# Kernel tuning notes

Measured on AMD Instinct MI355X. Metric: run time of the kernel, lower is better.

## Reference

```python
import jax, jax.numpy as jnp
import numpy as np

B, T, E, H, D = 4, 2048, 1024, 16, 64


def setup_inputs() -> dict:
    key = jax.random.key(0)
    k1, k2, k3, k4 = jax.random.split(key, 4)
    s = 1.0 / np.sqrt(E)
    return {
        "x": jax.random.normal(k1, (B, T, E), dtype=jnp.float32),
        "wj_w": jax.random.uniform(k2, (E, E), jnp.float32, -s, s),   # torch Linear weight (out,in)
        "wjv_w": jax.random.uniform(k3, (E, E), jnp.float32, -s, s),
        "wo_w": jax.random.uniform(k4, (E, H * D), jnp.float32, -s, s),
    }


def reference(x, wj_w, wjv_w, wo_w):
    b, t, e = x.shape
    # echo = x @ wj_w.T ; eb = echo @ wj_w  (F.linear with transposed weight)
    eb = (x @ wj_w.T) @ wj_w
    sc = jnp.sum(x * eb, axis=-1) / jnp.sqrt(jnp.asarray(e, x.dtype))  # (B,T)
    # rank-1 outer-product scores with strict-upper causal mask
    ja = sc[:, :, None] * sc[:, None, :]                               # (B,T,T)
    causal = jnp.tril(jnp.ones((t, t), dtype=bool))
    ja = jnp.where(causal[None], ja, -jnp.inf)
    ja = jax.nn.softmax(ja, axis=-1)                                   # (B,T,T)
    # values per head; attention map shared across heads (broadcast, not materialized)
    val = (x @ wjv_w.T).reshape(b, t, H, D)                            # (B,T,H,D)
    out = jnp.einsum("bts,bshd->bthd", ja, val)                       # (B,T,H,D)
    return out.reshape(b, t, H * D) @ wo_w.T                           # (B,T,E)
```

## Files before the change

kernel.cpp:

```cpp
#include <hip/hip_runtime.h>
#include <math.h>

#define R_ROWS 8192
#define T_SEQ  2048
#define E_DIM  1024
#define KC     32
#define KCR    256
#define PBATCH_ELEMS ((size_t)4352 * 512)

typedef __attribute__((ext_vector_type(8))) short short8;
typedef __attribute__((ext_vector_type(4))) float f32x4;

__device__ __forceinline__ ushort f2bf(float f) {
  uint u = __float_as_uint(f);
  u += 0x7FFFu + ((u >> 16) & 1u);
  return (ushort)(u >> 16);
}
__device__ __forceinline__ float bf2f(ushort h) {
  return __uint_as_float(((uint)h) << 16);
}


__global__ __launch_bounds__(256) void cvt_split_frag(
    const float* __restrict__ in, ushort* __restrict__ hi,
    ushort* __restrict__ lo, int n)
{
  int g = blockIdx.x * 256 + threadIdx.x;
  if (g >= n) return;
  const int l = g & 15, h = (g >> 4) & 3;
  const int pq = g >> 6;
  const int q = pq & (KC - 1), p = pq >> 5;
  const size_t src = (size_t)(p * 16 + l) * 1024 + q * 32 + h * 8;
  const float4 v0 = *(const float4*)&in[src];
  const float4 v1 = *(const float4*)&in[src + 4];
  ushort hh[8], ll[8];
  const float v[8] = {v0.x, v0.y, v0.z, v0.w, v1.x, v1.y, v1.z, v1.w};
#pragma unroll
  for (int e = 0; e < 8; ++e) {
    hh[e] = f2bf(v[e]);
    ll[e] = f2bf(v[e] - bf2f(hh[e]));
  }
  *(uint4*)&hi[(size_t)g * 8] = *(const uint4*)hh;
  *(uint4*)&lo[(size_t)g * 8] = *(const uint4*)ll;
}

__global__ __launch_bounds__(256) void cvt_splitT_frag(
    const float* __restrict__ in, ushort* __restrict__ hi,
    ushort* __restrict__ lo, int n)
{
  int g = blockIdx.x * 256 + threadIdx.x;
  if (g >= n) return;
  const int l = g & 15, h = (g >> 4) & 3;
  const int pq = g >> 6;
  const int q = pq & (KC - 1), p = pq >> 5;
  const int rr = p * 16 + l;
  const int cc = q * 32 + h * 8;
  ushort hh[8], ll[8];
#pragma unroll
  for (int e = 0; e < 8; ++e) {
    const float v = in[(size_t)(cc + e) * 1024 + rr];
    hh[e] = f2bf(v);
    ll[e] = f2bf(v - bf2f(hh[e]));
  }
  *(uint4*)&hi[(size_t)g * 8] = *(const uint4*)hh;
  *(uint4*)&lo[(size_t)g * 8] = *(const uint4*)ll;
}

struct Frags { short8 ah[4], al[4], bh[4], bl[4]; };

__global__ __launch_bounds__(256, 2) void gemm_sq_direct(
    const ushort* __restrict__ xh, const ushort* __restrict__ xl,
    const ushort* __restrict__ wh, const ushort* __restrict__ wl,
    float* __restrict__ sc_raw)
{
  const int tid = threadIdx.x;
  const int m0 = blockIdx.y * 128, n0 = blockIdx.x * 128;
  const int wave = tid >> 6, lane = tid & 63;
  const int l15 = lane & 15, lq = lane >> 4;
  const int wm = (wave & 1) * 64, wn = (wave >> 1) * 64;

  size_t aoff[4], boff[4];
#pragma unroll
  for (int i = 0; i < 4; ++i)
    aoff[i] = ((size_t)(((m0 + wm) >> 4) + i) * KC * 4 + lq) * 128 + l15 * 8;
#pragma unroll
  for (int j = 0; j < 4; ++j)
    boff[j] = ((size_t)(((n0 + wn) >> 4) + j) * KC * 4 + lq) * 128 + l15 * 8;

  f32x4 acc[4][4] = {};
  Frags f0, f1;

  auto load = [&](Frags& f, int q) {
    const size_t dq = (size_t)q * 512;
#pragma unroll
    for (int i = 0; i < 4; ++i) {
      f.ah[i] = *(const short8*)(xh + aoff[i] + dq);
      f.al[i] = *(const short8*)(xl + aoff[i] + dq);
    }
#pragma unroll
    for (int j = 0; j < 4; ++j) {
      f.bh[j] = *(const short8*)(wh + boff[j] + dq);
      f.bl[j] = *(const short8*)(wl + boff[j] + dq);
    }
  };
  auto step = [&](const Frags& f) {
#pragma unroll
    for (int i = 0; i < 4; ++i)
#pragma unroll
      for (int j = 0; j < 4; ++j) {
        acc[i][j] = __builtin_amdgcn_mfma_f32_16x16x32_bf16(f.ah[i], f.bh[j], acc[i][j], 0, 0, 0);
        acc[i][j] = __builtin_amdgcn_mfma_f32_16x16x32_bf16(f.ah[i], f.bl[j], acc[i][j], 0, 0, 0);
        acc[i][j] = __builtin_amdgcn_mfma_f32_16x16x32_bf16(f.al[i], f.bh[j], acc[i][j], 0, 0, 0);
      }
  };

  load(f0, 0);
#pragma unroll 1
  for (int q = 0; q < KC; q += 2) {
    load(f1, q + 1);
    step(f0);
    if (q + 2 < KC) load(f0, q + 2);
    step(f1);
  }

  __shared__ float red[128][33];
#pragma unroll
  for (int i = 0; i < 4; ++i)
#pragma unroll
    for (int r = 0; r < 4; ++r) {
      const int row = wm + i * 16 + lq * 4 + r;
      float s = 0.f;
#pragma unroll
      for (int j = 0; j < 4; ++j) s += acc[i][j][r] * acc[i][j][r];
      red[row][(l15 << 1) | (wave >> 1)] = s;
    }
  __syncthreads();
  if (tid < 128) {
    float s = 0.f;
#pragma unroll
    for (int c = 0; c < 32; ++c) s += red[tid][c];
    atomicAdd(&sc_raw[m0 + tid], s);
  }
}

struct Frags2 { short8 ah[2], al[2], bh[2], bl[2]; };

__global__ __launch_bounds__(256, 2) void gemm_m_split(
    const ushort* __restrict__ ah_, const ushort* __restrict__ al_,
    const ushort* __restrict__ bh_, const ushort* __restrict__ bl_,
    ushort* __restrict__ Mf)
{
  const int tid = threadIdx.x;
  const int m0 = blockIdx.y * 64, n0 = blockIdx.x * 64;
  const int wave = tid >> 6, lane = tid & 63;
  const int l15 = lane & 15, lq = lane >> 4;
  const int wm = (wave & 1) * 32, wn = (wave >> 1) * 32;

  size_t aoff[2], boff[2];
#pragma unroll
  for (int i = 0; i < 2; ++i)
    aoff[i] = ((size_t)(((m0 + wm) >> 4) + i) * KC * 4 + lq) * 128 + l15 * 8;
#pragma unroll
  for (int j = 0; j < 2; ++j)
    boff[j] = ((size_t)(((n0 + wn) >> 4) + j) * KC * 4 + lq) * 128 + l15 * 8;

  f32x4 acc[2][2] = {};
  Frags2 f0, f1;

  auto load = [&](Frags2& f, int q) {
    const size_t dq = (size_t)q * 512;
#pragma unroll
    for (int i = 0; i < 2; ++i) {
      f.ah[i] = *(const short8*)(ah_ + aoff[i] + dq);
      f.al[i] = *(const short8*)(al_ + aoff[i] + dq);
    }
#pragma unroll
    for (int j = 0; j < 2; ++j) {
      f.bh[j] = *(const short8*)(bh_ + boff[j] + dq);
      f.bl[j] = *(const short8*)(bl_ + boff[j] + dq);
    }
  };
  auto step = [&](const Frags2& f) {
#pragma unroll
    for (int i = 0; i < 2; ++i)
#pragma unroll
      for (int j = 0; j < 2; ++j) {
        acc[i][j] = __builtin_amdgcn_mfma_f32_16x16x32_bf16(f.ah[i], f.bh[j], acc[i][j], 0, 0, 0);
        acc[i][j] = __builtin_amdgcn_mfma_f32_16x16x32_bf16(f.ah[i], f.bl[j], acc[i][j], 0, 0, 0);
        acc[i][j] = __builtin_amdgcn_mfma_f32_16x16x32_bf16(f.al[i], f.bh[j], acc[i][j], 0, 0, 0);
      }
  };

  load(f0, 0);
#pragma unroll 1
  for (int q = 0; q < KC; q += 2) {
    load(f1, q + 1);
    step(f0);
    if (q + 2 < KC) load(f0, q + 2);
    step(f1);
  }

#pragma unroll
  for (int i = 0; i < 2; ++i)
#pragma unroll
    for (int j = 0; j < 2; ++j) {
      const int fb = m0 + wm + i * 16 + lq * 4;
      const int k  = n0 + wn + j * 16 + l15;
#pragma unroll
      for (int r = 0; r < 4; ++r) {
        const int f = fb + r;
        const size_t addr =
            (((size_t)(f >> 4) * KC + (k >> 5)) * 4 + ((k >> 3) & 3)) * 128 +
            (f & 15) * 8 + (k & 7);
        Mf[addr] = f2bf(acc[i][j][r]);
      }
    }
}

__global__ __launch_bounds__(1024) void scan_max(
    const float* __restrict__ sc_raw, float* __restrict__ sc,
    float* __restrict__ pmax)
{
  const int b = blockIdx.x;
  __shared__ float b0[T_SEQ];
  __shared__ float b1[T_SEQ];
  const int tid = threadIdx.x;
  for (int i = tid; i < T_SEQ; i += 1024) {
    const float v = sc_raw[b*T_SEQ + i] * 0.03125f;
    b0[i] = v;
    sc[b*T_SEQ + i] = v;
  }
  __syncthreads();
  float* src = b0; float* dst = b1;
  for (int off = 1; off < T_SEQ; off <<= 1) {
    for (int i = tid; i < T_SEQ; i += 1024)
      dst[i] = (i >= off) ? fmaxf(src[i], src[i - off]) : src[i];
    __syncthreads();
    float* tmp = src; src = dst; dst = tmp;
  }
  for (int i = tid; i < T_SEQ; i += 1024) pmax[b*T_SEQ + i] = src[i];
}

__global__ __launch_bounds__(256) void zgen(
    const float* __restrict__ sc, const float* __restrict__ pmax,
    float* __restrict__ zinv)
{
  const int row = blockIdx.x * 4 + (threadIdx.x >> 6);
  const int lane = threadIdx.x & 63;
  const int t = row & (T_SEQ - 1);
  const int base = row & ~(T_SEQ - 1);
  const float st = sc[row], pm = pmax[row];
  float z = 0.f;
  for (int s = lane; s <= t; s += 64)
    z += __expf(st * (sc[base + s] - pm));
#pragma unroll
  for (int m = 1; m < 64; m <<= 1) z += __shfl_xor(z, m);
  if (lane == 0) zinv[row] = 1.0f / z;
}

__global__ __launch_bounds__(512) void pgen(
    const float* __restrict__ sc, const float* __restrict__ pmax,
    ushort* __restrict__ P012, ushort* __restrict__ P3)
{
  const int y = blockIdx.x, b = blockIdx.y, zslice = blockIdx.z;
  const int bT = b * T_SEQ;
  ushort* pb = (b < 3) ? P012 + (size_t)b * PBATCH_ELEMS : P3;
  __shared__ float scs[T_SEQ];
  __shared__ float pms[T_SEQ];
  const int tid = threadIdx.x;
  for (int i = tid; i < T_SEQ; i += 512) {
    scs[i] = sc[bT + i];
    pms[i] = pmax[bT + i];
  }
  __syncthreads();

#pragma unroll 1
  for (int ph = 0; ph < 2; ++ph) {
    const int P = ph ? y : 15 - y;
    const int W = 4 * P + 4;
    ushort* base = pb + (size_t)(16 * P * (P + 1)) * 512;
    const int nu = 512 * W;
#pragma unroll 1
    for (int u = tid + zslice * 512; u < nu; u += 2048) {
      const int sub = u & 63, hi = sub >> 4, l = sub & 15;
      const int pr = (u >> 6) & 7, q = u >> 9;
      const int t = P * 128 + pr * 16 + l;
      const int s0 = q * 32 + hi * 8;
      const float st = scs[t], pm = pms[t];
      ushort tmp[8];
#pragma unroll
      for (int e = 0; e < 8; ++e) {
        const int s = s0 + e;
        float pe = 0.f;
        if (s <= t) pe = __expf(st * (scs[s] - pm));
        tmp[e] = f2bf(pe);
      }
      *(uint4*)&base[(size_t)(pr * W + q) * 512 + hi * 128 + l * 8] =
          *(const uint4*)tmp;
    }
  }
}

struct FragsP { short8 a[4], b[4]; };

__global__ __launch_bounds__(256, 2) void gemm_wt(
    const ushort* __restrict__ Af, const ushort* __restrict__ Bf,
    ushort* __restrict__ WT)
{
  const int tid = threadIdx.x;
  const int m0 = blockIdx.y * 128, n0 = blockIdx.x * 128;
  const int wave = tid >> 6, lane = tid & 63;
  const int l15 = lane & 15, lq = lane >> 4;
  const int wm = (wave & 1) * 64, wn = (wave >> 1) * 64;

  size_t aoff[4], boff[4];
#pragma unroll
  for (int i = 0; i < 4; ++i)
    aoff[i] = ((size_t)(((m0 + wm) >> 4) + i) * KC * 4 + lq) * 128 + l15 * 8;
#pragma unroll
  for (int j = 0; j < 4; ++j)
    boff[j] = ((size_t)(((n0 + wn) >> 4) + j) * KC * 4 + lq) * 128 + l15 * 8;

  f32x4 acc[4][4] = {};
  FragsP f0, f1;

  auto load = [&](FragsP& f, int q) {
    const size_t dq = (size_t)q * 512;
#pragma unroll
    for (int i = 0; i < 4; ++i) f.a[i] = *(const short8*)(Af + aoff[i] + dq);
#pragma unroll
    for (int j = 0; j < 4; ++j) f.b[j] = *(const short8*)(Bf + boff[j] + dq);
  };
  auto step = [&](const FragsP& f) {
#pragma unroll
    for (int i = 0; i < 4; ++i)
#pragma unroll
      for (int j = 0; j < 4; ++j)
        acc[i][j] = __builtin_amdgcn_mfma_f32_16x16x32_bf16(f.a[i], f.b[j], acc[i][j], 0, 0, 0);
  };

  load(f0, 0);
#pragma unroll 1
  for (int q = 0; q < KC; q += 2) {
    load(f1, q + 1);
    step(f0);
    if (q + 2 < KC) load(f0, q + 2);
    step(f1);
  }

#pragma unroll
  for (int i = 0; i < 4; ++i)
#pragma unroll
    for (int j = 0; j < 4; ++j) {
      const int eb = m0 + wm + i * 16 + lq * 4;
      const int rg = n0 + wn + j * 16 + l15;
#pragma unroll
      for (int r = 0; r < 4; ++r) {
        const int e = eb + r;
        const size_t addr =
            (((size_t)(e >> 4) * KCR + (rg >> 5)) * 4 + ((rg >> 3) & 3)) * 128 +
            (e & 15) * 8 + (rg & 7);
        WT[addr] = f2bf(acc[i][j][r]);
      }
    }
}

__global__ __launch_bounds__(256, 2) void attn_gemm(
    const ushort* __restrict__ P012, const ushort* __restrict__ P3,
    const ushort* __restrict__ WT, const float* __restrict__ zinv,
    float* __restrict__ outp)
{
  const int b = blockIdx.z, y = blockIdx.y;
  const int e0 = blockIdx.x * 128;
  const int bT = b * T_SEQ;
  const ushort* pb = (b < 3) ? P012 + (size_t)b * PBATCH_ELEMS : P3;
  const int tid = threadIdx.x;
  const int wave = tid >> 6, lane = tid & 63;
  const int l15 = lane & 15, lq = lane >> 4;
  const int wm = (wave & 1) * 64, wn = (wave >> 1) * 64;

  size_t boff[4];
#pragma unroll
  for (int j = 0; j < 4; ++j)
    boff[j] = ((size_t)((((e0 + wn) >> 4) + j) * KCR + (bT >> 5)) * 4 + lq) * 128
              + l15 * 8;

#pragma unroll 1
  for (int ph = 0; ph < 2; ++ph) {
    const int ty = ph ? y : 15 - y;
    const int W = 4 * ty + 4;
    const int t0 = ty * 128;

    size_t aoff[4];
#pragma unroll
    for (int i = 0; i < 4; ++i)
      aoff[i] = ((size_t)(16 * ty * (ty + 1)) + (size_t)((wm >> 4) + i) * W) * 512
                + lq * 128 + l15 * 8;

    f32x4 acc[4][4] = {};
    FragsP f0, f1;

    auto load = [&](FragsP& f, int q) {
      const size_t dq = (size_t)q * 512;
#pragma unroll
      for (int i = 0; i < 4; ++i) f.a[i] = *(const short8*)(pb + aoff[i] + dq);
#pragma unroll
      for (int j = 0; j < 4; ++j) f.b[j] = *(const short8*)(WT + boff[j] + dq);
    };
    auto step = [&](const FragsP& f) {
#pragma unroll
      for (int i = 0; i < 4; ++i)
#pragma unroll
        for (int j = 0; j < 4; ++j)
          acc[i][j] = __builtin_amdgcn_mfma_f32_16x16x32_bf16(f.a[i], f.b[j], acc[i][j], 0, 0, 0);
    };

    load(f0, 0);
#pragma unroll 1
    for (int q = 0; q < W; q += 2) {
      load(f1, q + 1);
      step(f0);
      if (q + 2 < W) load(f0, q + 2);
      step(f1);
    }

#pragma unroll
    for (int i = 0; i < 4; ++i)
#pragma unroll
      for (int r = 0; r < 4; ++r) {
        const int row = t0 + wm + i * 16 + lq * 4 + r;
        const float zi = zinv[bT + row];
#pragma unroll
        for (int j = 0; j < 4; ++j) {
          const int nb = e0 + wn + j * 16 + l15;
          outp[(size_t)(bT + row) * E_DIM + nb] = acc[i][j][r] * zi;
        }
      }
  }
}

extern "C" void kernel_launch(void* const* d_in, const int* in_sizes, int n_in,
                              void* d_out, int out_size, void* d_ws, size_t ws_size,
                              hipStream_t stream) {
  (void)in_sizes; (void)n_in; (void)out_size; (void)ws_size;
  const float* x   = (const float*)d_in[0];
  const float* wj  = (const float*)d_in[1];
  const float* wjv = (const float*)d_in[2];
  const float* wo  = (const float*)d_in[3];
  float* out = (float*)d_out;

  ushort* xh_f  = (ushort*)d_ws;
  ushort* xl_f  = xh_f  + (size_t)R_ROWS * E_DIM;
  ushort* bufA  = xl_f  + (size_t)R_ROWS * E_DIM;
  ushort* bufB  = bufA  + (size_t)E_DIM * E_DIM;
  ushort* bufC  = bufB  + (size_t)E_DIM * E_DIM;
  ushort* bufD  = bufC  + (size_t)E_DIM * E_DIM;
  ushort* Mf    = bufD  + (size_t)E_DIM * E_DIM;
  float* sc_raw = (float*)(Mf + (size_t)E_DIM * E_DIM);
  float* sc     = sc_raw + R_ROWS;
  float* pmax   = sc + R_ROWS;
  float* zinv   = pmax + R_ROWS;
  ushort* WT    = xl_f;
  ushort* P012  = xh_f;
  ushort* P3    = bufA;

  hipMemsetAsync(sc_raw, 0, R_ROWS * sizeof(float), stream);

  cvt_split_frag <<<E_DIM*E_DIM/8/256, 256, 0, stream>>>(wo,  bufA, bufB, E_DIM*E_DIM/8);
  cvt_splitT_frag<<<E_DIM*E_DIM/8/256, 256, 0, stream>>>(wjv, bufC, bufD, E_DIM*E_DIM/8);
  gemm_m_split<<<dim3(E_DIM/64, E_DIM/64), 256, 0, stream>>>(bufA, bufB, bufC, bufD, Mf);

  cvt_split_frag<<<R_ROWS*E_DIM/8/256, 256, 0, stream>>>(x,  xh_f, xl_f, R_ROWS*E_DIM/8);
  cvt_split_frag<<<E_DIM*E_DIM/8/256, 256, 0, stream>>>(wj, bufA, bufB, E_DIM*E_DIM/8);

  gemm_sq_direct<<<dim3(E_DIM/128, R_ROWS/128), 256, 0, stream>>>(
      xh_f, xl_f, bufA, bufB, sc_raw);
  scan_max<<<4, 1024, 0, stream>>>(sc_raw, sc, pmax);
  zgen<<<R_ROWS/4, 256, 0, stream>>>(sc, pmax, zinv);

  gemm_wt<<<dim3(R_ROWS/128, E_DIM/128), 256, 0, stream>>>(Mf, xh_f, WT);

  pgen<<<dim3(8, 4, 4), 512, 0, stream>>>(sc, pmax, P012, P3);

  attn_gemm<<<dim3(E_DIM/128, 8, 4), 256, 0, stream>>>(P012, P3, WT, zinv, out);
}
```

Before: 275.2 us.

## Fuse weight conversions into one launch and widen attention GEMM to eight waves

Merges the three weight bf16 hi/lo split kernels into a single launch, giving each weight its own workspace buffers. The attention GEMM block grows from 4 to 8 waves, with each wave computing a 64x32 tile instead of 64x64. This aims to cut launch overhead and raise latency hiding and occupancy in the final GEMM. The trade-offs are extra workspace and more redundant loads of the A fragments per MFMA.

```diff
diff --git a/kernel.cpp b/kernel.cpp
--- a/kernel.cpp
+++ b/kernel.cpp
@@ -21,12 +21,10 @@
 }
 
 
-__global__ __launch_bounds__(256) void cvt_split_frag(
+__device__ __forceinline__ void split_frag_unit(
     const float* __restrict__ in, ushort* __restrict__ hi,
-    ushort* __restrict__ lo, int n)
-{
-  int g = blockIdx.x * 256 + threadIdx.x;
-  if (g >= n) return;
+    ushort* __restrict__ lo, int g)
+{
   const int l = g & 15, h = (g >> 4) & 3;
   const int pq = g >> 6;
   const int q = pq & (KC - 1), p = pq >> 5;
@@ -44,12 +42,10 @@
   *(uint4*)&lo[(size_t)g * 8] = *(const uint4*)ll;
 }
 
-__global__ __launch_bounds__(256) void cvt_splitT_frag(
+__device__ __forceinline__ void splitT_frag_unit(
     const float* __restrict__ in, ushort* __restrict__ hi,
-    ushort* __restrict__ lo, int n)
-{
-  int g = blockIdx.x * 256 + threadIdx.x;
-  if (g >= n) return;
+    ushort* __restrict__ lo, int g)
+{
   const int l = g & 15, h = (g >> 4) & 3;
   const int pq = g >> 6;
   const int q = pq & (KC - 1), p = pq >> 5;
@@ -64,6 +60,29 @@
   }
   *(uint4*)&hi[(size_t)g * 8] = *(const uint4*)hh;
   *(uint4*)&lo[(size_t)g * 8] = *(const uint4*)ll;
+}
+
+__global__ __launch_bounds__(256) void cvt_split_frag(
+    const float* __restrict__ in, ushort* __restrict__ hi,
+    ushort* __restrict__ lo, int n)
+{
+  int g = blockIdx.x * 256 + threadIdx.x;
+  if (g >= n) return;
+  split_frag_unit(in, hi, lo, g);
+}
+
+__global__ __launch_bounds__(256) void cvt_weights(
+    const float* __restrict__ wo, const float* __restrict__ wjv,
+    const float* __restrict__ wj,
+    ushort* __restrict__ woh, ushort* __restrict__ wol,
+    ushort* __restrict__ wjvh, ushort* __restrict__ wjvl,
+    ushort* __restrict__ wjh, ushort* __restrict__ wjl)
+{
+  const int blk = blockIdx.x;
+  const int g = (blk & 511) * 256 + threadIdx.x;
+  if (blk < 512)            split_frag_unit (wo,  woh,  wol,  g);
+  else if (blk < 1024)      splitT_frag_unit(wjv, wjvh, wjvl, g);
+  else                      split_frag_unit (wj,  wjh,  wjl,  g);
 }
 
 struct Frags { short8 ah[4], al[4], bh[4], bl[4]; };
@@ -365,7 +384,9 @@
     }
 }
 
-__global__ __launch_bounds__(256, 2) void attn_gemm(
+struct Frags6 { short8 a[4], b[2]; };
+
+__global__ __launch_bounds__(512) void attn_gemm(
     const ushort* __restrict__ P012, const ushort* __restrict__ P3,
     const ushort* __restrict__ WT, const float* __restrict__ zinv,
     float* __restrict__ outp)
@@ -377,11 +398,12 @@
   const int tid = threadIdx.x;
   const int wave = tid >> 6, lane = tid & 63;
   const int l15 = lane & 15, lq = lane >> 4;
-  const int wm = (wave & 1) * 64, wn = (wave >> 1) * 64;
-
-  size_t boff[4];
-#pragma unroll
-  for (int j = 0; j < 4; ++j)
+  const int wm = (wave & 1) * 64;
+  const int wn = (wave >> 1) * 32;
+
+  size_t boff[2];
+#pragma unroll
+  for (int j = 0; j < 2; ++j)
     boff[j] = ((size_t)((((e0 + wn) >> 4) + j) * KCR + (bT >> 5)) * 4 + lq) * 128
               + l15 * 8;
 
@@ -397,21 +419,21 @@
       aoff[i] = ((size_t)(16 * ty * (ty + 1)) + (size_t)((wm >> 4) + i) * W) * 512
                 + lq * 128 + l15 * 8;
 
-    f32x4 acc[4][4] = {};
-    FragsP f0, f1;
-
-    auto load = [&](FragsP& f, int q) {
+    f32x4 acc[4][2] = {};
+    Frags6 f0, f1;
+
+    auto load = [&](Frags6& f, int q) {
       const size_t dq = (size_t)q * 512;
 #pragma unroll
       for (int i = 0; i < 4; ++i) f.a[i] = *(const short8*)(pb + aoff[i] + dq);
 #pragma unroll
-      for (int j = 0; j < 4; ++j) f.b[j] = *(const short8*)(WT + boff[j] + dq);
+      for (int j = 0; j < 2; ++j) f.b[j] = *(const short8*)(WT + boff[j] + dq);
     };
-    auto step = [&](const FragsP& f) {
+    auto step = [&](const Frags6& f) {
 #pragma unroll
       for (int i = 0; i < 4; ++i)
 #pragma unroll
-        for (int j = 0; j < 4; ++j)
+        for (int j = 0; j < 2; ++j)
           acc[i][j] = __builtin_amdgcn_mfma_f32_16x16x32_bf16(f.a[i], f.b[j], acc[i][j], 0, 0, 0);
     };
 
@@ -431,7 +453,7 @@
         const int row = t0 + wm + i * 16 + lq * 4 + r;
         const float zi = zinv[bT + row];
 #pragma unroll
-        for (int j = 0; j < 4; ++j) {
+        for (int j = 0; j < 2; ++j) {
           const int nb = e0 + wn + j * 16 + l15;
           outp[(size_t)(bT + row) * E_DIM + nb] = acc[i][j][r] * zi;
         }
@@ -451,30 +473,34 @@
 
   ushort* xh_f  = (ushort*)d_ws;
   ushort* xl_f  = xh_f  + (size_t)R_ROWS * E_DIM;
-  ushort* bufA  = xl_f  + (size_t)R_ROWS * E_DIM;
-  ushort* bufB  = bufA  + (size_t)E_DIM * E_DIM;
-  ushort* bufC  = bufB  + (size_t)E_DIM * E_DIM;
-  ushort* bufD  = bufC  + (size_t)E_DIM * E_DIM;
-  ushort* Mf    = bufD  + (size_t)E_DIM * E_DIM;
+  ushort* woh   = xl_f  + (size_t)R_ROWS * E_DIM;
+  ushort* wol   = woh   + (size_t)E_DIM * E_DIM;
+  ushort* wjvh  = wol   + (size_t)E_DIM * E_DIM;
+  ushort* wjvl  = wjvh  + (size_t)E_DIM * E_DIM;
+  ushort* wjh   = wjvl  + (size_t)E_DIM * E_DIM;
+  ushort* wjl   = wjh   + (size_t)E_DIM * E_DIM;
+  ushort* Mf    = wjl   + (size_t)E_DIM * E_DIM;
   float* sc_raw = (float*)(Mf + (size_t)E_DIM * E_DIM);
   float* sc     = sc_raw + R_ROWS;
   float* pmax   = sc + R_ROWS;
   float* zinv   = pmax + R_ROWS;
   ushort* WT    = xl_f;
   ushort* P012  = xh_f;
-  ushort* P3    = bufA;
+  ushort* P3    = woh;
 
   hipMemsetAsync(sc_raw, 0, R_ROWS * sizeof(float), stream);
 
-  cvt_split_frag <<<E_DIM*E_DIM/8/256, 256, 0, stream>>>(wo,  bufA, bufB, E_DIM*E_DIM/8);
-  cvt_splitT_frag<<<E_DIM*E_DIM/8/256, 256, 0, stream>>>(wjv, bufC, bufD, E_DIM*E_DIM/8);
-  gemm_m_split<<<dim3(E_DIM/64, E_DIM/64), 256, 0, stream>>>(bufA, bufB, bufC, bufD, Mf);
-
-  cvt_split_frag<<<R_ROWS*E_DIM/8/256, 256, 0, stream>>>(x,  xh_f, xl_f, R_ROWS*E_DIM/8);
-  cvt_split_frag<<<E_DIM*E_DIM/8/256, 256, 0, stream>>>(wj, bufA, bufB, E_DIM*E_DIM/8);
+  cvt_weights<<<1536, 256, 0, stream>>>(wo, wjv, wj,
+                                        woh, wol, wjvh, wjvl, wjh, wjl);
+
+  gemm_m_split<<<dim3(E_DIM/64, E_DIM/64), 256, 0, stream>>>(
+      woh, wol, wjvh, wjvl, Mf);
+
+  cvt_split_frag<<<R_ROWS*E_DIM/8/256, 256, 0, stream>>>(
+      x, xh_f, xl_f, R_ROWS*E_DIM/8);
 
   gemm_sq_direct<<<dim3(E_DIM/128, R_ROWS/128), 256, 0, stream>>>(
-      xh_f, xl_f, bufA, bufB, sc_raw);
+      xh_f, xl_f, wjh, wjl, sc_raw);
   scan_max<<<4, 1024, 0, stream>>>(sc_raw, sc, pmax);
   zgen<<<R_ROWS/4, 256, 0, stream>>>(sc, pmax, zinv);
 
@@ -482,5 +508,5 @@
 
   pgen<<<dim3(8, 4, 4), 512, 0, stream>>>(sc, pmax, P012, P3);
 
-  attn_gemm<<<dim3(E_DIM/128, 8, 4), 256, 0, stream>>>(P012, P3, WT, zinv, out);
-}
+  attn_gemm<<<dim3(E_DIM/128, 8, 4), 512, 0, stream>>>(P012, P3, WT, zinv, out);
+}
```

New measurement: 268.3 us. 2.5% less time.

## Fuse conversions, scan and normalizer into fewer kernels; unpair attention tiles

Applied to the files above, without the earlier changes.

The four fp32-to-bf16 hi/lo split conversions and the memset are merged into one launch, `cvt_all`. The scan_max and zgen kernels are removed. `pgen2` now recomputes the prefix max per block and accumulates the softmax normalizer with shuffle reductions plus float atomics while it generates P. `attn_gemm` no longer processes a balanced pair of row tiles per block; it launches one block per row tile and computes the reciprocal normalizer inline. The aim is to cut launch count and the extra full-sequence exp pass in zgen, at the cost of redundant prefix-scan work in every pgen block, atomic contention, and possible load imbalance across attention tiles.

```diff
diff --git a/kernel.cpp b/kernel.cpp
--- a/kernel.cpp
+++ b/kernel.cpp
@@ -21,12 +21,10 @@
 }
 
 
-__global__ __launch_bounds__(256) void cvt_split_frag(
+__device__ __forceinline__ void split_frag_unit(
     const float* __restrict__ in, ushort* __restrict__ hi,
-    ushort* __restrict__ lo, int n)
-{
-  int g = blockIdx.x * 256 + threadIdx.x;
-  if (g >= n) return;
+    ushort* __restrict__ lo, int g)
+{
   const int l = g & 15, h = (g >> 4) & 3;
   const int pq = g >> 6;
   const int q = pq & (KC - 1), p = pq >> 5;
@@ -44,12 +42,10 @@
   *(uint4*)&lo[(size_t)g * 8] = *(const uint4*)ll;
 }
 
-__global__ __launch_bounds__(256) void cvt_splitT_frag(
+__device__ __forceinline__ void splitT_frag_unit(
     const float* __restrict__ in, ushort* __restrict__ hi,
-    ushort* __restrict__ lo, int n)
-{
-  int g = blockIdx.x * 256 + threadIdx.x;
-  if (g >= n) return;
+    ushort* __restrict__ lo, int g)
+{
   const int l = g & 15, h = (g >> 4) & 3;
   const int pq = g >> 6;
   const int q = pq & (KC - 1), p = pq >> 5;
@@ -66,6 +62,33 @@
   *(uint4*)&lo[(size_t)g * 8] = *(const uint4*)ll;
 }
 
+__global__ __launch_bounds__(256) void cvt_all(
+    const float* __restrict__ x, const float* __restrict__ wo,
+    const float* __restrict__ wjv, const float* __restrict__ wj,
+    ushort* __restrict__ xh, ushort* __restrict__ xl,
+    ushort* __restrict__ woh, ushort* __restrict__ wol,
+    ushort* __restrict__ wjvh, ushort* __restrict__ wjvl,
+    ushort* __restrict__ wjh, ushort* __restrict__ wjl,
+    float* __restrict__ sc_raw, float* __restrict__ zsum)
+{
+  const int blk = blockIdx.x;
+  const int tid = threadIdx.x;
+  if (blk < 64) {
+    const int idx = blk * 256 + tid;
+    if (idx < R_ROWS) sc_raw[idx] = 0.f;
+    else              zsum[idx - R_ROWS] = 0.f;
+  }
+  if (blk < 4096) {
+    split_frag_unit(x, xh, xl, blk * 256 + tid);
+  } else if (blk < 4608) {
+    split_frag_unit(wo, woh, wol, (blk - 4096) * 256 + tid);
+  } else if (blk < 5120) {
+    splitT_frag_unit(wjv, wjvh, wjvl, (blk - 4608) * 256 + tid);
+  } else {
+    split_frag_unit(wj, wjh, wjl, (blk - 5120) * 256 + tid);
+  }
+}
+
 struct Frags { short8 ah[4], al[4], bh[4], bl[4]; };
 
 __global__ __launch_bounds__(256, 2) void gemm_sq_direct(
@@ -217,62 +240,34 @@
     }
 }
 
-__global__ __launch_bounds__(1024) void scan_max(
-    const float* __restrict__ sc_raw, float* __restrict__ sc,
-    float* __restrict__ pmax)
-{
-  const int b = blockIdx.x;
-  __shared__ float b0[T_SEQ];
-  __shared__ float b1[T_SEQ];
-  const int tid = threadIdx.x;
-  for (int i = tid; i < T_SEQ; i += 1024) {
-    const float v = sc_raw[b*T_SEQ + i] * 0.03125f;
-    b0[i] = v;
-    sc[b*T_SEQ + i] = v;
-  }
-  __syncthreads();
-  float* src = b0; float* dst = b1;
-  for (int off = 1; off < T_SEQ; off <<= 1) {
-    for (int i = tid; i < T_SEQ; i += 1024)
-      dst[i] = (i >= off) ? fmaxf(src[i], src[i - off]) : src[i];
-    __syncthreads();
-    float* tmp = src; src = dst; dst = tmp;
-  }
-  for (int i = tid; i < T_SEQ; i += 1024) pmax[b*T_SEQ + i] = src[i];
-}
-
-__global__ __launch_bounds__(256) void zgen(
-    const float* __restrict__ sc, const float* __restrict__ pmax,
-    float* __restrict__ zinv)
-{
-  const int row = blockIdx.x * 4 + (threadIdx.x >> 6);
-  const int lane = threadIdx.x & 63;
-  const int t = row & (T_SEQ - 1);
-  const int base = row & ~(T_SEQ - 1);
-  const float st = sc[row], pm = pmax[row];
-  float z = 0.f;
-  for (int s = lane; s <= t; s += 64)
-    z += __expf(st * (sc[base + s] - pm));
-#pragma unroll
-  for (int m = 1; m < 64; m <<= 1) z += __shfl_xor(z, m);
-  if (lane == 0) zinv[row] = 1.0f / z;
-}
-
-__global__ __launch_bounds__(512) void pgen(
-    const float* __restrict__ sc, const float* __restrict__ pmax,
-    ushort* __restrict__ P012, ushort* __restrict__ P3)
+__global__ __launch_bounds__(512) void pgen2(
+    const float* __restrict__ sc_raw, ushort* __restrict__ P012,
+    ushort* __restrict__ P3, float* __restrict__ zsum)
 {
   const int y = blockIdx.x, b = blockIdx.y, zslice = blockIdx.z;
   const int bT = b * T_SEQ;
   ushort* pb = (b < 3) ? P012 + (size_t)b * PBATCH_ELEMS : P3;
   __shared__ float scs[T_SEQ];
-  __shared__ float pms[T_SEQ];
+  __shared__ float pma[T_SEQ];
+  __shared__ float pmb[T_SEQ];
   const int tid = threadIdx.x;
   for (int i = tid; i < T_SEQ; i += 512) {
-    scs[i] = sc[bT + i];
-    pms[i] = pmax[bT + i];
+    const float v = sc_raw[bT + i] * 0.03125f;
+    scs[i] = v;
+    pma[i] = v;
   }
   __syncthreads();
+  float* src = pma; float* dst = pmb;
+  for (int off = 1; off < T_SEQ; off <<= 1) {
+    for (int i = tid; i < T_SEQ; i += 512)
+      dst[i] = (i >= off) ? fmaxf(src[i], src[i - off]) : src[i];
+    __syncthreads();
+    float* t = src; src = dst; dst = t;
+  }
+  const float* pms = src;
+
+  const int lane = tid & 63;
+  const int hi = lane >> 4, l = lane & 15;
 
 #pragma unroll 1
   for (int ph = 0; ph < 2; ++ph) {
@@ -282,21 +277,25 @@
     const int nu = 512 * W;
 #pragma unroll 1
     for (int u = tid + zslice * 512; u < nu; u += 2048) {
-      const int sub = u & 63, hi = sub >> 4, l = sub & 15;
       const int pr = (u >> 6) & 7, q = u >> 9;
       const int t = P * 128 + pr * 16 + l;
       const int s0 = q * 32 + hi * 8;
       const float st = scs[t], pm = pms[t];
       ushort tmp[8];
+      float z = 0.f;
 #pragma unroll
       for (int e = 0; e < 8; ++e) {
         const int s = s0 + e;
         float pe = 0.f;
         if (s <= t) pe = __expf(st * (scs[s] - pm));
         tmp[e] = f2bf(pe);
+        z += pe;
       }
       *(uint4*)&base[(size_t)(pr * W + q) * 512 + hi * 128 + l * 8] =
           *(const uint4*)tmp;
+      z += __shfl_xor(z, 16);
+      z += __shfl_xor(z, 32);
+      if (hi == 0) atomicAdd(&zsum[bT + t], z);
     }
   }
 }
@@ -367,76 +366,71 @@
 
 __global__ __launch_bounds__(256, 2) void attn_gemm(
     const ushort* __restrict__ P012, const ushort* __restrict__ P3,
-    const ushort* __restrict__ WT, const float* __restrict__ zinv,
+    const ushort* __restrict__ WT, const float* __restrict__ zsum,
     float* __restrict__ outp)
 {
-  const int b = blockIdx.z, y = blockIdx.y;
+  const int b = blockIdx.z;
+  const int ty = 15 - (int)blockIdx.y;
   const int e0 = blockIdx.x * 128;
   const int bT = b * T_SEQ;
   const ushort* pb = (b < 3) ? P012 + (size_t)b * PBATCH_ELEMS : P3;
   const int tid = threadIdx.x;
   const int wave = tid >> 6, lane = tid & 63;
   const int l15 = lane & 15, lq = lane >> 4;
-  const int wm = (wave & 1) * 64, wn = (wave >> 1) * 64;
-
-  size_t boff[4];
+  const int wm = (wave & 1) * 64;
+  const int wn = (wave >> 1) * 64;
+  const int W = 4 * ty + 4;
+  const int t0 = ty * 128;
+
+  size_t aoff[4], boff[4];
+#pragma unroll
+  for (int i = 0; i < 4; ++i)
+    aoff[i] = ((size_t)(16 * ty * (ty + 1)) + (size_t)((wm >> 4) + i) * W) * 512
+              + lq * 128 + l15 * 8;
 #pragma unroll
   for (int j = 0; j < 4; ++j)
     boff[j] = ((size_t)((((e0 + wn) >> 4) + j) * KCR + (bT >> 5)) * 4 + lq) * 128
               + l15 * 8;
 
-#pragma unroll 1
-  for (int ph = 0; ph < 2; ++ph) {
-    const int ty = ph ? y : 15 - y;
-    const int W = 4 * ty + 4;
-    const int t0 = ty * 128;
-
-    size_t aoff[4];
+  f32x4 acc[4][4] = {};
+  FragsP f0, f1;
+
+  auto load = [&](FragsP& f, int q) {
+    const size_t dq = (size_t)q * 512;
+#pragma unroll
+    for (int i = 0; i < 4; ++i) f.a[i] = *(const short8*)(pb + aoff[i] + dq);
+#pragma unroll
+    for (int j = 0; j < 4; ++j) f.b[j] = *(const short8*)(WT + boff[j] + dq);
+  };
+  auto step = [&](const FragsP& f) {
 #pragma unroll
     for (int i = 0; i < 4; ++i)
-      aoff[i] = ((size_t)(16 * ty * (ty + 1)) + (size_t)((wm >> 4) + i) * W) * 512
-                + lq * 128 + l15 * 8;
-
-    f32x4 acc[4][4] = {};
-    FragsP f0, f1;
-
-    auto load = [&](FragsP& f, int q) {
-      const size_t dq = (size_t)q * 512;
-#pragma unroll
-      for (int i = 0; i < 4; ++i) f.a[i] = *(const short8*)(pb + aoff[i] + dq);
-#pragma unroll
-      for (int j = 0; j < 4; ++j) f.b[j] = *(const short8*)(WT + boff[j] + dq);
-    };
-    auto step = [&](const FragsP& f) {
-#pragma unroll
-      for (int i = 0; i < 4; ++i)
-#pragma unroll
-        for (int j = 0; j < 4; ++j)
-          acc[i][j] = __builtin_amdgcn_mfma_f32_16x16x32_bf16(f.a[i], f.b[j], acc[i][j], 0, 0, 0);
-    };
-
-    load(f0, 0);
-#pragma unroll 1
-    for (int q = 0; q < W; q += 2) {
-      load(f1, q + 1);
-      step(f0);
-      if (q + 2 < W) load(f0, q + 2);
-      step(f1);
-    }
-
-#pragma unroll
-    for (int i = 0; i < 4; ++i)
-#pragma unroll
-      for (int r = 0; r < 4; ++r) {
-        const int row = t0 + wm + i * 16 + lq * 4 + r;
-        const float zi = zinv[bT + row];
-#pragma unroll
-        for (int j = 0; j < 4; ++j) {
-          const int nb = e0 + wn + j * 16 + l15;
-          outp[(size_t)(bT + row) * E_DIM + nb] = acc[i][j][r] * zi;
-        }
-      }
-  }
+#pragma unroll
+      for (int j = 0; j < 4; ++j)
+        acc[i][j] = __builtin_amdgcn_mfma_f32_16x16x32_bf16(f.a[i], f.b[j], acc[i][j], 0, 0, 0);
+  };
+
+  load(f0, 0);
+#pragma unroll 1
+  for (int q = 0; q < W; q += 2) {
+    load(f1, q + 1);
+    step(f0);
+    if (q + 2 < W) load(f0, q + 2);
+    step(f1);
+  }
+
+#pragma unroll
+  for (int i = 0; i < 4; ++i)
+#pragma unroll
+    for (int r = 0; r < 4; ++r) {
+      const int row = t0 + wm + i * 16 + lq * 4 + r;
+      const float zi = 1.0f / zsum[bT + row];
+#pragma unroll
+      for (int j = 0; j < 4; ++j) {
+        const int nb = e0 + wn + j * 16 + l15;
+        outp[(size_t)(bT + row) * E_DIM + nb] = acc[i][j][r] * zi;
+      }
+    }
 }
 
 extern "C" void kernel_launch(void* const* d_in, const int* in_sizes, int n_in,
@@ -451,36 +445,32 @@
 
   ushort* xh_f  = (ushort*)d_ws;
   ushort* xl_f  = xh_f  + (size_t)R_ROWS * E_DIM;
-  ushort* bufA  = xl_f  + (size_t)R_ROWS * E_DIM;
-  ushort* bufB  = bufA  + (size_t)E_DIM * E_DIM;
-  ushort* bufC  = bufB  + (size_t)E_DIM * E_DIM;
-  ushort* bufD  = bufC  + (size_t)E_DIM * E_DIM;
-  ushort* Mf    = bufD  + (size_t)E_DIM * E_DIM;
+  ushort* woh   = xl_f  + (size_t)R_ROWS * E_DIM;
+  ushort* wol   = woh   + (size_t)E_DIM * E_DIM;
+  ushort* wjvh  = wol   + (size_t)E_DIM * E_DIM;
+  ushort* wjvl  = wjvh  + (size_t)E_DIM * E_DIM;
+  ushort* wjh   = wjvl  + (size_t)E_DIM * E_DIM;
+  ushort* wjl   = wjh   + (size_t)E_DIM * E_DIM;
+  ushort* Mf    = wjl   + (size_t)E_DIM * E_DIM;
   float* sc_raw = (float*)(Mf + (size_t)E_DIM * E_DIM);
-  float* sc     = sc_raw + R_ROWS;
-  float* pmax   = sc + R_ROWS;
-  float* zinv   = pmax + R_ROWS;
+  float* zsum   = sc_raw + R_ROWS;
   ushort* WT    = xl_f;
   ushort* P012  = xh_f;
-  ushort* P3    = bufA;
-
-  hipMemsetAsync(sc_raw, 0, R_ROWS * sizeof(float), stream);
-
-  cvt_split_frag <<<E_DIM*E_DIM/8/256, 256, 0, stream>>>(wo,  bufA, bufB, E_DIM*E_DIM/8);
-  cvt_splitT_frag<<<E_DIM*E_DIM/8/256, 256, 0, stream>>>(wjv, bufC, bufD, E_DIM*E_DIM/8);
-  gemm_m_split<<<dim3(E_DIM/64, E_DIM/64), 256, 0, stream>>>(bufA, bufB, bufC, bufD, Mf);
-
-  cvt_split_frag<<<R_ROWS*E_DIM/8/256, 256, 0, stream>>>(x,  xh_f, xl_f, R_ROWS*E_DIM/8);
-  cvt_split_frag<<<E_DIM*E_DIM/8/256, 256, 0, stream>>>(wj, bufA, bufB, E_DIM*E_DIM/8);
+  ushort* P3    = woh;
+
+  cvt_all<<<5632, 256, 0, stream>>>(x, wo, wjv, wj,
+                                    xh_f, xl_f, woh, wol, wjvh, wjvl, wjh, wjl,
+                                    sc_raw, zsum);
+
+  gemm_m_split<<<dim3(E_DIM/64, E_DIM/64), 256, 0, stream>>>(
+      woh, wol, wjvh, wjvl, Mf);
 
   gemm_sq_direct<<<dim3(E_DIM/128, R_ROWS/128), 256, 0, stream>>>(
-      xh_f, xl_f, bufA, bufB, sc_raw);
-  scan_max<<<4, 1024, 0, stream>>>(sc_raw, sc, pmax);
-  zgen<<<R_ROWS/4, 256, 0, stream>>>(sc, pmax, zinv);
+      xh_f, xl_f, wjh, wjl, sc_raw);
 
   gemm_wt<<<dim3(R_ROWS/128, E_DIM/128), 256, 0, stream>>>(Mf, xh_f, WT);
 
-  pgen<<<dim3(8, 4, 4), 512, 0, stream>>>(sc, pmax, P012, P3);
-
-  attn_gemm<<<dim3(E_DIM/128, 8, 4), 256, 0, stream>>>(P012, P3, WT, zinv, out);
-}
+  pgen2<<<dim3(8, 4, 4), 512, 0, stream>>>(sc_raw, P012, P3, zsum);
+
+  attn_gemm<<<dim3(E_DIM/128, 16, 4), 256, 0, stream>>>(P012, P3, WT, zsum, out);
+}
```

Result: no change. 269.8 us (-1.9%).
